# Performance work log

Measured on AMD Instinct MI355X. Metric: run time of the kernel, lower is better.

The kernel has to match this reference:

```python
import jax, jax.numpy as jnp
import numpy as np

CHANNEL = 256
MEM_SIZE = 684
POS_NUM = 128
NEG_NUM = 512
TEMP = 1.0
CLASS_NUM = 60
BANK_ROWS = MEM_SIZE * CLASS_NUM  # 41040
BATCH = 512


def setup_inputs() -> dict:
    key = jax.random.key(0)
    k1, k2, k3, k4 = jax.random.split(key, 4)
    f = jax.random.normal(k1, (BATCH, CHANNEL), dtype=jnp.float32)
    f_normed = f / jnp.linalg.norm(f, axis=-1, keepdims=True)
    label = jax.random.randint(k2, (BATCH,), 0, CLASS_NUM, dtype=jnp.int32)
    bank = jax.random.normal(k3, (BANK_ROWS, CHANNEL), dtype=jnp.float32)
    bank = bank / jnp.linalg.norm(bank, axis=-1, keepdims=True)
    bank_flag = jnp.ones((BANK_ROWS,), dtype=jnp.float32)  # warmed-up bank
    rand_neg = jax.random.uniform(k4, (BATCH, BANK_ROWS), dtype=jnp.float32)
    # exact torch roundrobin enqueue logic (sequential over the batch)
    rr = np.zeros(CLASS_NUM, dtype=np.int64)
    idxs = []
    for i in np.asarray(label).tolist():
        rr[i] = rr[i] + 1 if rr[i] < CLASS_NUM - 1 else 0
        idxs.append(int(rr[i]) + i * MEM_SIZE)
    enqueue_idx = jnp.asarray(idxs, dtype=jnp.int32)
    return {"f_normed": f_normed, "label": label, "enqueue_idx": enqueue_idx,
            "bank": bank, "bank_flag": bank_flag, "rand_neg": rand_neg}


def reference(f_normed, label, enqueue_idx, bank, bank_flag, rand_neg):
    N = f_normed.shape[0]
    # enqueue (detached write, as in torch: Bank[indies] = f_normed.detach())
    bank = bank.at[enqueue_idx].set(jax.lax.stop_gradient(f_normed))
    flag = bank_flag.at[enqueue_idx].set(1.0)
    # all_pairs: [N, M]
    all_pairs = jnp.einsum('nc,mc->nm', f_normed, bank)
    bank_label = jnp.tile(jnp.arange(CLASS_NUM), MEM_SIZE)  # arange(C).repeat(mem)
    eq = label[:, None] == bank_label[None, :]
    valid = flag > 0
    pos_mask = eq & valid
    neg_mask = (~eq) & valid
    # hard positives: smallest POS_NUM positive similarities per row
    pos_hard = jnp.sort(jnp.where(pos_mask, all_pairs, jnp.inf), axis=-1)[:, :POS_NUM]
    # hard negatives: largest NEG_NUM negative similarities per row
    neg_hard, _ = jax.lax.top_k(jnp.where(neg_mask, all_pairs, -jnp.inf), NEG_NUM)
    # random negatives: uniform sample without replacement via noise argsort
    r = jnp.where(neg_mask, rand_neg, jnp.inf)
    rand_idx = jnp.argsort(r, axis=-1)[:, :NEG_NUM]
    neg_rand = jnp.take_along_axis(all_pairs, rand_idx, axis=-1)
    # combined logits: [N, 2*POS_NUM, 1+NEG_NUM]
    pos = pos_hard[:, :, None]
    h2h = jnp.concatenate([pos, jnp.broadcast_to(neg_hard[:, None, :], (N, POS_NUM, NEG_NUM))], axis=-1)
    h2r = jnp.concatenate([pos, jnp.broadcast_to(neg_rand[:, None, :], (N, POS_NUM, NEG_NUM))], axis=-1)
    combined = jnp.concatenate([h2h, h2r], axis=1).reshape(-1, 1 + NEG_NUM)
    # cross entropy with target class 0 for every row
    loss = -jnp.mean(jax.nn.log_softmax(combined / TEMP, axis=-1)[:, 0])
    return loss
```

## Files before the change

kernel.cpp:

```cpp
#include <hip/hip_runtime.h>

#define CH    256
#define MEM   684
#define POSN  128
#define NEGN  512
#define CLS   60
#define ROWS  41040
#define BATCHN 512

typedef unsigned int u32;
typedef unsigned short u16;
typedef unsigned long long u64;

typedef __attribute__((ext_vector_type(8))) short bf16x8;
typedef __attribute__((ext_vector_type(4))) float f32x4;

__device__ __forceinline__ float b2f(u16 u) { return __uint_as_float(((u32)u) << 16); }
__device__ __forceinline__ u16 f2b(float x) {
  u32 u = __float_as_uint(x);
  u32 r = ((u >> 16) & 1u) + 0x7FFFu;
  return (u16)((u + r) >> 16);
}
__device__ __forceinline__ u32 umin2(u32 a, u32 b) { return a < b ? a : b; }

#if defined(__has_builtin)
#if __has_builtin(__builtin_amdgcn_global_load_lds)
#define HAVE_GLL 1
#endif
#endif

__device__ __forceinline__ void stage16(const u16* g, u16* l) {
#ifdef HAVE_GLL
  __builtin_amdgcn_global_load_lds((const __attribute__((address_space(1))) void*)g,
                                   (__attribute__((address_space(3))) void*)l, 16, 0, 0);
#else
  *(uint4*)l = *(const uint4*)g;
#endif
}

__global__ __launch_bounds__(256) void k_convert(const float* __restrict__ bank,
                                                 u16* __restrict__ bankB) {
  size_t i = (size_t)(blockIdx.x * 256 + threadIdx.x) * 8;
  float4 a = *(const float4*)(bank + i);
  float4 b = *(const float4*)(bank + i + 4);
  uint4 o;
  o.x = (u32)f2b(a.x) | ((u32)f2b(a.y) << 16);
  o.y = (u32)f2b(a.z) | ((u32)f2b(a.w) << 16);
  o.z = (u32)f2b(b.x) | ((u32)f2b(b.y) << 16);
  o.w = (u32)f2b(b.z) | ((u32)f2b(b.w) << 16);
  *(uint4*)(bankB + i) = o;
}

__global__ __launch_bounds__(256) void k_scatter(const float* __restrict__ f,
                                                 const int* __restrict__ enq,
                                                 u16* __restrict__ fB,
                                                 u16* __restrict__ bankB) {
  int n = blockIdx.x, t = threadIdx.x;
  u16 v = f2b(f[n * CH + t]);
  fB[n * CH + t] = v;
  int row = enq[n];
  bankB[(size_t)row * CH + t] = v;
}

__global__ __launch_bounds__(256) void k_gemm(const u16* __restrict__ fB,
                                              const u16* __restrict__ bankB,
                                              u16* __restrict__ Cb) {
  __shared__ __align__(16) u16 As[128 * 32];
  __shared__ __align__(16) u16 Bs[128 * 32];
  const int tid = threadIdx.x;
  const int wave = tid >> 6, lane = tid & 63;
  const int bm = blockIdx.x * 128;
  const int bn = blockIdx.y * 128;
  const int wm = (wave & 1) * 64, wn = (wave >> 1) * 64;
  const int m_in = lane & 15;
  const int ks = (lane >> 4) * 8;

  f32x4 acc[4][4] = {};

  for (int k0 = 0; k0 < CH; k0 += 32) {
    __syncthreads();
#pragma unroll
    for (int i = 0; i < 2; i++) {
      int u = tid + 256 * i;
      int row = u >> 2;
      int kk = (u & 3) * 8;
      stage16(fB + (size_t)(bm + row) * CH + k0 + kk, As + u * 8);
      int rb = bn + row;
      if (rb >= ROWS) rb = bn;
      stage16(bankB + (size_t)rb * CH + k0 + kk, Bs + u * 8);
    }
    __syncthreads();

    bf16x8 af[4], bf[4];
#pragma unroll
    for (int t4 = 0; t4 < 4; t4++) {
      af[t4] = *(const bf16x8*)(As + (wm + t4 * 16 + m_in) * 32 + ks);
      bf[t4] = *(const bf16x8*)(Bs + (wn + t4 * 16 + m_in) * 32 + ks);
    }
#pragma unroll
    for (int mi = 0; mi < 4; mi++)
#pragma unroll
      for (int ni = 0; ni < 4; ni++)
        acc[mi][ni] = __builtin_amdgcn_mfma_f32_16x16x32_bf16(af[mi], bf[ni], acc[mi][ni], 0, 0, 0);
  }

  const int rr = (lane >> 4) * 4;
  const int cc = lane & 15;
#pragma unroll
  for (int mi = 0; mi < 4; mi++) {
#pragma unroll
    for (int ni = 0; ni < 4; ni++) {
      int ncol = bn + wn + ni * 16 + cc;
      if (ncol < ROWS) {
        size_t base = (size_t)(bm + wm + mi * 16 + rr) * ROWS + ncol;
#pragma unroll
        for (int q = 0; q < 4; q++) Cb[base + (size_t)q * ROWS] = f2b(acc[mi][ni][q]);
      }
    }
  }
}

__device__ __forceinline__ u32 scanN(u32 v, u32* tmp, int tid) {
  tmp[tid] = v;
  __syncthreads();
  for (int off = 1; off < 1024; off <<= 1) {
    u32 t = (tid >= off) ? tmp[tid - off] : 0u;
    __syncthreads();
    tmp[tid] += t;
    __syncthreads();
  }
  return tmp[tid];
}

__device__ __forceinline__ float redsum1024(float v, float* tmp, int tid) {
  tmp[tid] = v;
  __syncthreads();
  for (int off = 512; off > 0; off >>= 1) {
    if (tid < off) tmp[tid] += tmp[tid + off];
    __syncthreads();
  }
  float r = tmp[0];
  __syncthreads();
  return r;
}

__device__ __forceinline__ int binof(float v, float lo, float scale) {
  int b = (int)((v - lo) * scale);
  return b < 0 ? 0 : (b > 2047 ? 2047 : b);
}

__device__ __forceinline__ u32 wave_append(u32* cnt, bool pred) {
  u64 mask = __ballot(pred);
  u32 ret = 0xFFFFFFFFu;
  if (pred) {
    int lane = (int)(threadIdx.x & 63);
    int leader = __ffsll((u64)mask) - 1;
    u32 base = 0;
    if (lane == leader) base = atomicAdd(cnt, (u32)__popcll(mask));
    base = __shfl(base, leader, 64);
    ret = base + (u32)__popcll(mask & ((1ull << lane) - 1ull));
  }
  return ret;
}

#define VITER 5
#define VTAIL 80
#define VTAILBASE 40960
#define CAPC 3072
#define CAPR 1536

__global__ __launch_bounds__(1024) void k_select(const u16* __restrict__ Cb,
                                                 const float* __restrict__ rnd,
                                                 const int* __restrict__ label,
                                                 float* __restrict__ partial) {
  const int n = blockIdx.x;
  const int tid = threadIdx.x;
  const u16* crow = Cb + (size_t)n * ROWS;
  const float* rrow = rnd + (size_t)n * ROWS;
  const int lab = label[n];

  __shared__ __align__(16) char smem[56448];
  u32* histc = (u32*)(smem);
  u32* histr = (u32*)(smem + 8192);
  float* clist = (float*)(smem + 16384);
  float* rl_rv = (float*)(smem + 28672);
  float* rl_cv = (float*)(smem + 34816);
  u32* rl_mi = (u32*)(smem + 40960);
  u32* stmp = (u32*)(smem + 47104);
  float* fred = (float*)(smem + 47104);
  float* cb_c = (float*)(smem + 51200);
  float* rb_r = (float*)(smem + 53248);
  float* rb_c = (float*)(smem + 54272);
  u32* rb_m = (u32*)(smem + 55296);
  u32* ctl = (u32*)(smem + 56320);
  float* bc_f = (float*)(ctl + 8);
  float* posv = clist;

  const int rv0 = (tid * 8) % 60;

  float T1 = 0.09375f;
  float T0 = 0.03125f;
  u32 F = 0, G = 0;
  float sc_c, sc_r;

  for (int attempt = 0;; attempt++) {
    for (int i = tid; i < 2048; i += 1024) { histc[i] = 0; histr[i] = 0; }
    if (tid == 0) { ctl[0] = 0; ctl[1] = 0; }
    __syncthreads();
    sc_c = 2048.0f / (1.0625f - T1);
    sc_r = 2048.0f / T0;
    int rb = rv0;
    for (int it = 0; it < VITER; it++) {
      int m8 = (it * 1024 + tid) * 8;
      uint4 cr = *(const uint4*)(crow + m8);
      float4 ra = *(const float4*)(rrow + m8);
      float4 rb4 = *(const float4*)(rrow + m8 + 4);
      u32 cw[4] = {cr.x, cr.y, cr.z, cr.w};
      float rs[8] = {ra.x, ra.y, ra.z, ra.w, rb4.x, rb4.y, rb4.z, rb4.w};
      int r = rb;
#pragma unroll
      for (int j = 0; j < 8; j++) {
        bool isneg = (r != lab);
        float c = b2f((u16)(cw[j >> 1] >> ((j & 1) * 16)));
        bool pc = isneg && (c > T1);
        u32 p1 = wave_append(&ctl[0], pc);
        if (pc) {
          if (p1 < CAPC) clist[p1] = c;
          atomicAdd(&histc[binof(c, T1, sc_c)], 1u);
        }
        float rv = rs[j];
        bool pr = isneg && (rv < T0);
        u32 p2 = wave_append(&ctl[1], pr);
        if (pr) {
          if (p2 < CAPR) { rl_rv[p2] = rv; rl_cv[p2] = c; rl_mi[p2] = (u32)(m8 + j); }
          atomicAdd(&histr[binof(rv, 0.0f, sc_r)], 1u);
        }
        r++;
        if (r == 60) r = 0;
      }
      rb += 32;
      if (rb >= 60) rb -= 60;
    }
    if (tid < VTAIL) {
      int m = VTAILBASE + tid;
      int r = 40 + tid;
      if (r >= 60) r -= 60;
      bool isneg = (r != lab);
      float c = b2f(crow[m]);
      bool pc = isneg && (c > T1);
      u32 p1 = wave_append(&ctl[0], pc);
      if (pc) {
        if (p1 < CAPC) clist[p1] = c;
        atomicAdd(&histc[binof(c, T1, sc_c)], 1u);
      }
      float rv = rrow[m];
      bool pr = isneg && (rv < T0);
      u32 p2 = wave_append(&ctl[1], pr);
      if (pr) {
        if (p2 < CAPR) { rl_rv[p2] = rv; rl_cv[p2] = c; rl_mi[p2] = (u32)m; }
        atomicAdd(&histr[binof(rv, 0.0f, sc_r)], 1u);
      }
    }
    __syncthreads();
    F = ctl[0];
    G = ctl[1];
    __syncthreads();
    if (F >= NEGN && G >= NEGN) break;
    if (F < NEGN) T1 = -1.1f;
    if (G < NEGN) T0 = 1.1f;
  }
  const bool listc_ok = (F <= CAPC);
  const bool listr_ok = (G <= CAPR);

  if (tid == 0) { ctl[2] = 0; ctl[3] = 0; ctl[4] = 0; ctl[5] = 0; ctl[6] = 0; ctl[7] = 0; }
  u32 fsum = histc[tid * 2] + histc[tid * 2 + 1];
  u32 finc = scanN(fsum, stmp, tid);
  u32 fexc = finc - fsum;
  u32 tcpos = F - NEGN + 1;
  if (fexc < tcpos && tcpos <= finc) {
    u32 run = fexc;
#pragma unroll
    for (int i = 0; i < 2; i++) {
      u32 h = histc[tid * 2 + i];
      if (run + h >= tcpos) { ctl[4] = (u32)(tid * 2 + i); ctl[5] = F - (run + h); break; }
      run += h;
    }
  }
  __syncthreads();
  const u32 b_c = ctl[4], cnt_gt = ctl[5];

  u32 gsum = histr[tid * 2] + histr[tid * 2 + 1];
  u32 ginc = scanN(gsum, stmp, tid);
  u32 gexc = ginc - gsum;
  if (gexc < NEGN && NEGN <= ginc) {
    u32 run = gexc;
#pragma unroll
    for (int i = 0; i < 2; i++) {
      u32 h = histr[tid * 2 + i];
      if (run + h >= NEGN) { ctl[6] = (u32)(tid * 2 + i); ctl[7] = run; break; }
      run += h;
    }
  }
  __syncthreads();
  const u32 b_r = ctl[6], cnt_lt = ctl[7];
  const u32 need_c = NEGN - cnt_gt;
  const u32 need_r = NEGN - cnt_lt;

  float sH = 0.f, sR = 0.f;
  if (listc_ok) {
    for (u32 i = tid; i < F; i += 1024) {
      float c = clist[i];
      u32 b = (u32)binof(c, T1, sc_c);
      if (b > b_c) sH += expf(c);
      else if (b == b_c) {
        u32 id = atomicAdd(&ctl[2], 1u);
        if (id < 512) cb_c[id] = c;
      }
    }
  }
  if (listr_ok) {
    for (u32 i = tid; i < G; i += 1024) {
      float rv = rl_rv[i];
      u32 b = (u32)binof(rv, 0.0f, sc_r);
      if (b < b_r) sR += expf(rl_cv[i]);
      else if (b == b_r) {
        u32 id = atomicAdd(&ctl[3], 1u);
        if (id < 256) { rb_r[id] = rv; rb_c[id] = rl_cv[i]; rb_m[id] = rl_mi[i]; }
      }
    }
  }
  if (!listc_ok || !listr_ok) {
    for (int m = tid; m < ROWS; m += 1024) {
      int r = m % 60;
      if (r == lab) continue;
      float c = b2f(crow[m]);
      if (!listc_ok && c > T1) {
        u32 b = (u32)binof(c, T1, sc_c);
        if (b > b_c) sH += expf(c);
        else if (b == b_c) {
          u32 id = atomicAdd(&ctl[2], 1u);
          if (id < 512) cb_c[id] = c;
        }
      }
      if (!listr_ok) {
        float rv = rrow[m];
        if (rv < T0) {
          u32 b = (u32)binof(rv, 0.0f, sc_r);
          if (b < b_r) sR += expf(c);
          else if (b == b_r) {
            u32 id = atomicAdd(&ctl[3], 1u);
            if (id < 256) { rb_r[id] = rv; rb_c[id] = c; rb_m[id] = (u32)m; }
          }
        }
      }
    }
  }
  __syncthreads();
  float SHsum = redsum1024(sH, fred, tid);
  float SRsum = redsum1024(sR, fred, tid);

  if (tid == 0) {
    float addH = 0.f;
    u32 Lc = umin2(ctl[2], 512u);
    u32 kc = umin2(need_c, Lc);
    for (u32 k = 0; k < kc; k++) {
      int best = 0;
      float bv = -3.0e38f;
      for (u32 i = 0; i < Lc; i++)
        if (cb_c[i] > bv) { bv = cb_c[i]; best = (int)i; }
      cb_c[best] = -3.0e38f;
      addH += expf(bv);
    }
    u32 Lr = umin2(ctl[3], 256u);
    for (u32 i = 1; i < Lr; i++) {
      float rv = rb_r[i]; u32 mm = rb_m[i]; float cv = rb_c[i];
      int j = (int)i - 1;
      while (j >= 0 && (rb_r[j] > rv || (rb_r[j] == rv && rb_m[j] > mm))) {
        rb_r[j + 1] = rb_r[j]; rb_m[j + 1] = rb_m[j]; rb_c[j + 1] = rb_c[j];
        j--;
      }
      rb_r[j + 1] = rv; rb_m[j + 1] = mm; rb_c[j + 1] = cv;
    }
    float addR = 0.f;
    u32 kr = umin2(need_r, Lr);
    for (u32 i = 0; i < kr; i++) addR += expf(rb_c[i]);
    bc_f[0] = addH;
    bc_f[1] = addR;
  }
  __syncthreads();
  const float S_H = SHsum + bc_f[0];
  const float S_R = SRsum + bc_f[1];
  __syncthreads();

  posv[tid] = (tid < MEM) ? b2f(crow[lab + CLS * tid]) : INFINITY;
  __syncthreads();
  for (u32 k = 2; k <= 1024; k <<= 1) {
    for (u32 j = k >> 1; j > 0; j >>= 1) {
      u32 i = (u32)tid;
      u32 ix = i ^ j;
      if (ix > i) {
        float a = posv[i], b = posv[ix];
        bool up = ((i & k) == 0);
        if ((a > b) == up) { posv[i] = b; posv[ix] = a; }
      }
      __syncthreads();
    }
  }

  float term = 0.f;
  if (tid < POSN) {
    float p = posv[tid];
    float e = expf(p);
    term = (p - logf(e + S_H)) + (p - logf(e + S_R));
  }
  float tot = redsum1024(term, fred, tid);
  if (tid == 0) partial[n] = tot;
}

__global__ __launch_bounds__(256) void k_final(const float* __restrict__ partial,
                                               float* __restrict__ out) {
  __shared__ float fred[256];
  int tid = threadIdx.x;
  float v = partial[tid] + partial[tid + 256];
  fred[tid] = v;
  __syncthreads();
  for (int off = 128; off > 0; off >>= 1) {
    if (tid < off) fred[tid] += fred[tid + off];
    __syncthreads();
  }
  if (tid == 0) out[0] = -fred[0] / (float)(BATCHN * 2 * POSN);
}

extern "C" void kernel_launch(void* const* d_in, const int* in_sizes, int n_in,
                              void* d_out, int out_size, void* d_ws, size_t ws_size,
                              hipStream_t stream) {
  const float* f = (const float*)d_in[0];
  const int* label = (const int*)d_in[1];
  const int* enq = (const int*)d_in[2];
  const float* bank = (const float*)d_in[3];
  const float* rnd = (const float*)d_in[5];
  float* out = (float*)d_out;

  char* ws = (char*)d_ws;
  u16* bankB = (u16*)ws;
  u16* fB = (u16*)(ws + 21012480);
  u16* Cb = (u16*)(ws + 21012480 + 262144);
  float* partial = (float*)(ws + 21012480 + 262144 + 42024960);

  k_convert<<<dim3(5130), dim3(256), 0, stream>>>(bank, bankB);
  k_scatter<<<dim3(BATCHN), dim3(256), 0, stream>>>(f, enq, fB, bankB);
  k_gemm<<<dim3(4, 321), dim3(256), 0, stream>>>(fB, bankB, Cb);
  k_select<<<dim3(BATCHN), dim3(1024), 0, stream>>>(Cb, rnd, label, partial);
  k_final<<<dim3(1), dim3(256), 0, stream>>>(partial, out);
}
```

Baseline: 245.1 us.

## Use wave-level scans and batched appends, replace positive bitonic sort with histogram select

Replaces the per-element ballot append with a per-thread count followed by one wave prefix scan and one atomic per wave. The barrier-heavy 1024-thread LDS scan and reduction become shuffle-based wave scans and reductions. The 1024-element bitonic sort of positives is replaced by a histogram threshold select, with a serial selection pass over the boundary bin on thread 0. This cuts many __syncthreads and LDS round trips, but adds a second pass over candidates and a serial tail on one thread that could be slow when many values fall in the boundary bin.

```diff
diff --git a/kernel.cpp b/kernel.cpp
--- a/kernel.cpp
+++ b/kernel.cpp
@@ -120,25 +120,53 @@
   }
 }
 
-__device__ __forceinline__ u32 scanN(u32 v, u32* tmp, int tid) {
-  tmp[tid] = v;
-  __syncthreads();
-  for (int off = 1; off < 1024; off <<= 1) {
-    u32 t = (tid >= off) ? tmp[tid - off] : 0u;
-    __syncthreads();
-    tmp[tid] += t;
-    __syncthreads();
-  }
-  return tmp[tid];
+__device__ __forceinline__ u32 wscan_incl(u32 v) {
+  int lane = (int)(threadIdx.x & 63);
+#pragma unroll
+  for (int off = 1; off < 64; off <<= 1) {
+    u32 t = __shfl_up(v, off, 64);
+    if (lane >= off) v += t;
+  }
+  return v;
+}
+
+__device__ __forceinline__ u32 wave_multi_append(u32* cnt, u32 nc) {
+  u32 inc = wscan_incl(nc);
+  u32 base = 0;
+  if ((threadIdx.x & 63) == 63) base = atomicAdd(cnt, inc);
+  base = __shfl(base, 63, 64);
+  return base + inc - nc;
+}
+
+__device__ __forceinline__ u32 scan1024(u32 v, u32* tmp, int tid) {
+  u32 inc = wscan_incl(v);
+  int wid = tid >> 6;
+  if ((tid & 63) == 63) tmp[wid] = inc;
+  __syncthreads();
+  if (tid < 64) {
+    u32 t = (tid < 16) ? tmp[tid] : 0u;
+    u32 ti = wscan_incl(t);
+    if (tid < 16) tmp[tid] = ti - t;
+  }
+  __syncthreads();
+  u32 r = inc + tmp[wid];
+  __syncthreads();
+  return r;
 }
 
 __device__ __forceinline__ float redsum1024(float v, float* tmp, int tid) {
-  tmp[tid] = v;
-  __syncthreads();
-  for (int off = 512; off > 0; off >>= 1) {
-    if (tid < off) tmp[tid] += tmp[tid + off];
-    __syncthreads();
-  }
+#pragma unroll
+  for (int off = 32; off > 0; off >>= 1) v += __shfl_xor(v, off, 64);
+  int wid = tid >> 6;
+  if ((tid & 63) == 0) tmp[wid] = v;
+  __syncthreads();
+  if (tid == 0) {
+    float t = 0.f;
+#pragma unroll
+    for (int i = 0; i < 16; i++) t += tmp[i];
+    tmp[0] = t;
+  }
+  __syncthreads();
   float r = tmp[0];
   __syncthreads();
   return r;
@@ -147,20 +175,6 @@
 __device__ __forceinline__ int binof(float v, float lo, float scale) {
   int b = (int)((v - lo) * scale);
   return b < 0 ? 0 : (b > 2047 ? 2047 : b);
-}
-
-__device__ __forceinline__ u32 wave_append(u32* cnt, bool pred) {
-  u64 mask = __ballot(pred);
-  u32 ret = 0xFFFFFFFFu;
-  if (pred) {
-    int lane = (int)(threadIdx.x & 63);
-    int leader = __ffsll((u64)mask) - 1;
-    u32 base = 0;
-    if (lane == leader) base = atomicAdd(cnt, (u32)__popcll(mask));
-    base = __shfl(base, leader, 64);
-    ret = base + (u32)__popcll(mask & ((1ull << lane) - 1ull));
-  }
-  return ret;
 }
 
 #define VITER 5
@@ -169,10 +183,10 @@
 #define CAPC 3072
 #define CAPR 1536
 
-__global__ __launch_bounds__(1024) void k_select(const u16* __restrict__ Cb,
-                                                 const float* __restrict__ rnd,
-                                                 const int* __restrict__ label,
-                                                 float* __restrict__ partial) {
+__global__ __launch_bounds__(1024, 8) void k_select(const u16* __restrict__ Cb,
+                                                    const float* __restrict__ rnd,
+                                                    const int* __restrict__ label,
+                                                    float* __restrict__ partial) {
   const int n = blockIdx.x;
   const int tid = threadIdx.x;
   const u16* crow = Cb + (size_t)n * ROWS;
@@ -194,7 +208,6 @@
   u32* rb_m = (u32*)(smem + 55296);
   u32* ctl = (u32*)(smem + 56320);
   float* bc_f = (float*)(ctl + 8);
-  float* posv = clist;
 
   const int rv0 = (tid * 8) % 60;
 
@@ -217,23 +230,36 @@
       float4 rb4 = *(const float4*)(rrow + m8 + 4);
       u32 cw[4] = {cr.x, cr.y, cr.z, cr.w};
       float rs[8] = {ra.x, ra.y, ra.z, ra.w, rb4.x, rb4.y, rb4.z, rb4.w};
+      float cv_[8];
+      u32 nc = 0, nr = 0;
       int r = rb;
 #pragma unroll
       for (int j = 0; j < 8; j++) {
         bool isneg = (r != lab);
         float c = b2f((u16)(cw[j >> 1] >> ((j & 1) * 16)));
-        bool pc = isneg && (c > T1);
-        u32 p1 = wave_append(&ctl[0], pc);
-        if (pc) {
-          if (p1 < CAPC) clist[p1] = c;
+        cv_[j] = c;
+        nc += (isneg && c > T1) ? 1u : 0u;
+        nr += (isneg && rs[j] < T0) ? 1u : 0u;
+        r++;
+        if (r == 60) r = 0;
+      }
+      u32 s1 = wave_multi_append(&ctl[0], nc);
+      u32 s2 = wave_multi_append(&ctl[1], nr);
+      r = rb;
+#pragma unroll
+      for (int j = 0; j < 8; j++) {
+        bool isneg = (r != lab);
+        float c = cv_[j];
+        if (isneg && c > T1) {
+          if (s1 < CAPC) clist[s1] = c;
           atomicAdd(&histc[binof(c, T1, sc_c)], 1u);
+          s1++;
         }
         float rv = rs[j];
-        bool pr = isneg && (rv < T0);
-        u32 p2 = wave_append(&ctl[1], pr);
-        if (pr) {
-          if (p2 < CAPR) { rl_rv[p2] = rv; rl_cv[p2] = c; rl_mi[p2] = (u32)(m8 + j); }
+        if (isneg && rv < T0) {
+          if (s2 < CAPR) { rl_rv[s2] = rv; rl_cv[s2] = c; rl_mi[s2] = (u32)(m8 + j); }
           atomicAdd(&histr[binof(rv, 0.0f, sc_r)], 1u);
+          s2++;
         }
         r++;
         if (r == 60) r = 0;
@@ -241,23 +267,28 @@
       rb += 32;
       if (rb >= 60) rb -= 60;
     }
-    if (tid < VTAIL) {
+    {
+      const bool act = tid < VTAIL;
+      float c = 0.f, rv = 1.f;
+      bool pc = false, pr = false;
       int m = VTAILBASE + tid;
-      int r = 40 + tid;
-      if (r >= 60) r -= 60;
-      bool isneg = (r != lab);
-      float c = b2f(crow[m]);
-      bool pc = isneg && (c > T1);
-      u32 p1 = wave_append(&ctl[0], pc);
+      if (act) {
+        int r = 40 + tid;
+        if (r >= 60) r -= 60;
+        bool isneg = (r != lab);
+        c = b2f(crow[m]);
+        rv = rrow[m];
+        pc = isneg && (c > T1);
+        pr = isneg && (rv < T0);
+      }
+      u32 s1 = wave_multi_append(&ctl[0], pc ? 1u : 0u);
+      u32 s2 = wave_multi_append(&ctl[1], pr ? 1u : 0u);
       if (pc) {
-        if (p1 < CAPC) clist[p1] = c;
+        if (s1 < CAPC) clist[s1] = c;
         atomicAdd(&histc[binof(c, T1, sc_c)], 1u);
       }
-      float rv = rrow[m];
-      bool pr = isneg && (rv < T0);
-      u32 p2 = wave_append(&ctl[1], pr);
       if (pr) {
-        if (p2 < CAPR) { rl_rv[p2] = rv; rl_cv[p2] = c; rl_mi[p2] = (u32)m; }
+        if (s2 < CAPR) { rl_rv[s2] = rv; rl_cv[s2] = c; rl_mi[s2] = (u32)m; }
         atomicAdd(&histr[binof(rv, 0.0f, sc_r)], 1u);
       }
     }
@@ -274,7 +305,7 @@
 
   if (tid == 0) { ctl[2] = 0; ctl[3] = 0; ctl[4] = 0; ctl[5] = 0; ctl[6] = 0; ctl[7] = 0; }
   u32 fsum = histc[tid * 2] + histc[tid * 2 + 1];
-  u32 finc = scanN(fsum, stmp, tid);
+  u32 finc = scan1024(fsum, stmp, tid);
   u32 fexc = finc - fsum;
   u32 tcpos = F - NEGN + 1;
   if (fexc < tcpos && tcpos <= finc) {
@@ -290,7 +321,7 @@
   const u32 b_c = ctl[4], cnt_gt = ctl[5];
 
   u32 gsum = histr[tid * 2] + histr[tid * 2 + 1];
-  u32 ginc = scanN(gsum, stmp, tid);
+  u32 ginc = scan1024(gsum, stmp, tid);
   u32 gexc = ginc - gsum;
   if (gexc < NEGN && NEGN <= ginc) {
     u32 run = gexc;
@@ -392,29 +423,63 @@
   const float S_R = SRsum + bc_f[1];
   __syncthreads();
 
-  posv[tid] = (tid < MEM) ? b2f(crow[lab + CLS * tid]) : INFINITY;
-  __syncthreads();
-  for (u32 k = 2; k <= 1024; k <<= 1) {
-    for (u32 j = k >> 1; j > 0; j >>= 1) {
-      u32 i = (u32)tid;
-      u32 ix = i ^ j;
-      if (ix > i) {
-        float a = posv[i], b = posv[ix];
-        bool up = ((i & k) == 0);
-        if ((a > b) == up) { posv[i] = b; posv[ix] = a; }
-      }
-      __syncthreads();
-    }
-  }
-
+  float pval = 0.f;
+  int pbin = 0;
+  const bool hasp = tid < MEM;
+  const float PLO = -1.03125f;
+  const float PSC = 2048.0f / 2.09375f;
+  if (hasp) {
+    pval = b2f(crow[lab + CLS * tid]);
+    pbin = binof(pval, PLO, PSC);
+  }
+  for (int i = tid; i < 2048; i += 1024) histc[i] = 0;
+  if (tid == 0) { ctl[2] = 0; ctl[4] = 0; ctl[5] = 0; }
+  __syncthreads();
+  if (hasp) atomicAdd(&histc[pbin], 1u);
+  __syncthreads();
+  u32 hsum = histc[tid * 2] + histc[tid * 2 + 1];
+  u32 hinc = scan1024(hsum, stmp, tid);
+  u32 hexc = hinc - hsum;
+  if (hexc < POSN && POSN <= hinc) {
+    u32 run = hexc;
+#pragma unroll
+    for (int i = 0; i < 2; i++) {
+      u32 h = histc[tid * 2 + i];
+      if (run + h >= POSN) { ctl[4] = (u32)(tid * 2 + i); ctl[5] = run; break; }
+      run += h;
+    }
+  }
+  __syncthreads();
+  const u32 b_p = ctl[4], cnt_below = ctl[5];
+  const u32 need_p = POSN - cnt_below;
+  if (hasp && (u32)pbin == b_p) {
+    u32 id = atomicAdd(&ctl[2], 1u);
+    if (id < 512) cb_c[id] = pval;
+  }
   float term = 0.f;
-  if (tid < POSN) {
-    float p = posv[tid];
-    float e = expf(p);
-    term = (p - logf(e + S_H)) + (p - logf(e + S_R));
-  }
+  if (hasp && (u32)pbin < b_p) {
+    float e = expf(pval);
+    term = (pval - logf(e + S_H)) + (pval - logf(e + S_R));
+  }
+  __syncthreads();
+  if (tid == 0) {
+    u32 L = umin2(ctl[2], 512u);
+    u32 kp = umin2(need_p, L);
+    float add = 0.f;
+    for (u32 k = 0; k < kp; k++) {
+      int best = 0;
+      float bv = 3.0e38f;
+      for (u32 i = 0; i < L; i++)
+        if (cb_c[i] < bv) { bv = cb_c[i]; best = (int)i; }
+      cb_c[best] = 3.0e38f;
+      float e = expf(bv);
+      add += (bv - logf(e + S_H)) + (bv - logf(e + S_R));
+    }
+    bc_f[0] = add;
+  }
+  __syncthreads();
   float tot = redsum1024(term, fred, tid);
-  if (tid == 0) partial[n] = tot;
+  if (tid == 0) partial[n] = tot + bc_f[0];
 }
 
 __global__ __launch_bounds__(256) void k_final(const float* __restrict__ partial,
```

Measured after the change: 237.2 us. 3.2% less time.
